# Kernel optimization log

Hardware: AMD Instinct MI355X
Metric: run time of the kernel (lower is better)

Reference implementation:

```python
import jax, jax.numpy as jnp
import numpy as np

B, S, EMB, H = 4, 1024, 1024, 16
HD = EMB // H          # head_dim = 64
MAXP = 512             # RelativePositionalEncoder default max_position


def setup_inputs() -> dict:
    key = jax.random.key(0)
    ks = jax.random.split(key, 13)
    s = 1.0 / np.sqrt(EMB)  # xavier-ish scale keeps softmax logits sane
    return {
        "query": jax.random.normal(ks[0], (B, S, EMB), jnp.float32),
        "key": jax.random.normal(ks[1], (B, S, EMB), jnp.float32),
        "value": jax.random.normal(ks[2], (B, S, EMB), jnp.float32),
        "Wq": jax.random.normal(ks[3], (EMB, EMB), jnp.float32) * s,
        "bq": jnp.zeros((EMB,), jnp.float32),
        "Wk": jax.random.normal(ks[4], (EMB, EMB), jnp.float32) * s,
        "bk": jnp.zeros((EMB,), jnp.float32),
        "Wv": jax.random.normal(ks[5], (EMB, EMB), jnp.float32) * s,
        "bv": jnp.zeros((EMB,), jnp.float32),
        "Wo": jax.random.normal(ks[6], (EMB, EMB), jnp.float32) * s,
        "bo": jnp.zeros((EMB,), jnp.float32),
        "rel_k": jax.random.normal(ks[7], (2 * MAXP + 1, HD), jnp.float32) * 0.05,
        "rel_v": jax.random.normal(ks[8], (2 * MAXP + 1, HD), jnp.float32) * 0.05,
    }


def _split_heads(x):
    # [B,S,E] -> [B,S,H,HD] -> [B,H,S,HD] -> [B*H,S,HD]
    return x.reshape(B, S, H, HD).transpose(0, 2, 1, 3).reshape(B * H, S, HD)


def reference(query, key, value, Wq, bq, Wk, bk, Wv, bv, Wo, bo, rel_k, rel_v):
    scale = jnp.sqrt(jnp.asarray(HD, query.dtype))
    q = _split_heads(query @ Wq + bq)
    k = _split_heads(key @ Wk + bk)
    v = _split_heads(value @ Wv + bv)
    # relative position lookup tables: [Sq, Sk, HD]
    rp = jnp.clip(jnp.arange(S)[None, :] - jnp.arange(S)[:, None], -MAXP, MAXP) + MAXP
    a_key = rel_k[rp]
    a_value = rel_v[rp]
    qk = jnp.einsum('bqd,bkd->bqk', q, k)              # [B*H,S,S]
    rel_qk = jnp.einsum('bqd,qkd->bqk', q, a_key)      # relative score term
    attn = jax.nn.softmax((qk + rel_qk) / scale, axis=-1)
    out = jnp.einsum('bqk,bkd->bqd', attn, v) + jnp.einsum('bqk,qkd->bqd', attn, a_value)
    # faithful to original's view(num_heads, batch, -1, head_dim) then concat reshape
    out = out.reshape(H, B, S, HD).transpose(0, 2, 1, 3).reshape(B, S, H * HD)
    out = out @ Wo + bo
    return (out, attn)
```

## Files before the change

kernel.cpp:

```cpp
#include <hip/hip_runtime.h>


using s16x8 = __attribute__((ext_vector_type(8))) short;
using f32x4 = __attribute__((ext_vector_type(4))) float;

#define MFMA16 __builtin_amdgcn_mfma_f32_16x16x32_bf16

__device__ __forceinline__ float bf2f(unsigned short u) {
  union { unsigned int u; float f; } v; v.u = ((unsigned int)u) << 16; return v.f;
}
__device__ __forceinline__ unsigned short f2bf(float f) {
  union { float f; unsigned int u; } v; v.f = f;
  unsigned int r = (v.u + 0x7FFFu + ((v.u >> 16) & 1u)) >> 16;
  return (unsigned short)r;
}

__global__ __launch_bounds__(256)
void k_prep(const float* __restrict__ Wq, const float* __restrict__ Wk,
            const float* __restrict__ Wv, const float* __restrict__ Wo,
            unsigned short* __restrict__ wqt, unsigned short* __restrict__ wkt,
            unsigned short* __restrict__ wvt, unsigned short* __restrict__ wot,
            const float* __restrict__ rk, const float* __restrict__ rv,
            unsigned short* __restrict__ relkb, unsigned short* __restrict__ rvTb) {
  const int b = blockIdx.x;
  const int tid = threadIdx.x;
  if (b < 4096) {
    __shared__ float t[32][33];
    const int sel = b >> 10, idx = b & 1023;
    const float* W = sel == 0 ? Wq : (sel == 1 ? Wk : (sel == 2 ? Wv : Wo));
    unsigned short* Wt = sel == 0 ? wqt : (sel == 1 ? wkt : (sel == 2 ? wvt : wot));
    const int n0 = (idx & 31) * 32, k0 = (idx >> 5) * 32;
    const int tx = tid & 31, ty = tid >> 5;
#pragma unroll
    for (int r = 0; r < 4; ++r)
      t[ty * 4 + r][tx] = W[(size_t)(k0 + ty * 4 + r) * 1024 + n0 + tx];
    __syncthreads();
#pragma unroll
    for (int r = 0; r < 4; ++r)
      Wt[(size_t)(n0 + ty * 4 + r) * 1024 + k0 + tx] = f2bf(t[tx][ty * 4 + r]);
  } else {
    const int b2 = b - 4096;
    if (b2 < 33) {
      int i = (b2 * 256 + tid) * 8;
      if (i < 65600) {
        float4 a = *(const float4*)(rk + i);
        float4 c = *(const float4*)(rk + i + 4);
        s16x8 o;
        o[0] = (short)f2bf(a.x); o[1] = (short)f2bf(a.y); o[2] = (short)f2bf(a.z); o[3] = (short)f2bf(a.w);
        o[4] = (short)f2bf(c.x); o[5] = (short)f2bf(c.y); o[6] = (short)f2bf(c.z); o[7] = (short)f2bf(c.w);
        *(s16x8*)(relkb + i) = o;
      }
    } else {
      int i = (b2 - 33) * 256 + tid;
      if (i < 65600) {
        int p = i >> 6, d = i & 63;
        rvTb[d * 1040 + p] = f2bf(rv[i]);
      }
    }
  }
}

__global__ __launch_bounds__(256)
void k_trV(const unsigned short* __restrict__ v, unsigned short* __restrict__ vt) {
  __shared__ unsigned short T[64][72];
  const int tid = threadIdx.x;
  const int bh = blockIdx.x >> 4;
  const int s0 = (blockIdx.x & 15) << 6;
  const int r = tid >> 2, cb = (tid & 3) << 4;
  const unsigned short* src = v + ((size_t)bh << 16) + (size_t)(s0 + r) * 64 + cb;
  *(s16x8*)&T[r][cb] = *(const s16x8*)src;
  *(s16x8*)&T[r][cb + 8] = *(const s16x8*)(src + 8);
  __syncthreads();
  unsigned short* dst = vt + ((size_t)bh << 16) + (size_t)r * 1024 + s0 + cb;
  s16x8 o0, o1;
#pragma unroll
  for (int e = 0; e < 8; ++e) o0[e] = T[cb + e][r];
#pragma unroll
  for (int e = 0; e < 8; ++e) o1[e] = T[cb + 8 + e][r];
  *(s16x8*)dst = o0;
  *(s16x8*)(dst + 8) = o1;
}

__global__ __launch_bounds__(256, 2)
void k_gemm_qkv(const float* __restrict__ Aq, const float* __restrict__ Ak, const float* __restrict__ Av,
                const unsigned short* __restrict__ Wq_, const unsigned short* __restrict__ Wk_,
                const unsigned short* __restrict__ Wv_,
                const float* __restrict__ bq_, const float* __restrict__ bk_, const float* __restrict__ bv_,
                unsigned short* __restrict__ Oq, unsigned short* __restrict__ Ok,
                unsigned short* __restrict__ Ov) {
  const int z = blockIdx.z;
  const float* A = z == 0 ? Aq : (z == 1 ? Ak : Av);
  const unsigned short* BT = z == 0 ? Wq_ : (z == 1 ? Wk_ : Wv_);
  const float* bias = z == 0 ? bq_ : (z == 1 ? bk_ : bv_);
  unsigned short* Cout = z == 0 ? Oq : (z == 1 ? Ok : Ov);

  __shared__ alignas(16) unsigned short aT[2][4096];
  __shared__ alignas(16) unsigned short bT[2][2048];
  const int tid = threadIdx.x;
  const int lane = tid & 63;
  const int l15 = lane & 15, lhi = lane >> 4;
  const int w = tid >> 6;
  const int wr = w * 32;
  const int brow = blockIdx.y * 128, bcol = blockIdx.x * 64;
  f32x4 acc[2][4] = {};

  const int c1 = tid, c2 = tid + 256;
  const int r1 = c1 >> 2, kA1 = (c1 & 3) * 8;
  const int r2 = c2 >> 2, kA2 = (c2 & 3) * 8;
  float4 a0, a1, a2, a3;
  s16x8 w1v, w2v;

#define LOADA(kt) do {                                                     \
    const float* p1 = A + (size_t)(brow + r1) * 1024 + (kt) * 32 + kA1;    \
    a0 = *(const float4*)p1; a1 = *(const float4*)(p1 + 4);                \
    const float* p2 = A + (size_t)(brow + r2) * 1024 + (kt) * 32 + kA2;    \
    a2 = *(const float4*)p2; a3 = *(const float4*)(p2 + 4);                \
  } while (0)
#define CVTA() do {                                                        \
    w1v[0] = (short)f2bf(a0.x); w1v[1] = (short)f2bf(a0.y);                \
    w1v[2] = (short)f2bf(a0.z); w1v[3] = (short)f2bf(a0.w);                \
    w1v[4] = (short)f2bf(a1.x); w1v[5] = (short)f2bf(a1.y);                \
    w1v[6] = (short)f2bf(a1.z); w1v[7] = (short)f2bf(a1.w);                \
    w2v[0] = (short)f2bf(a2.x); w2v[1] = (short)f2bf(a2.y);                \
    w2v[2] = (short)f2bf(a2.z); w2v[3] = (short)f2bf(a2.w);                \
    w2v[4] = (short)f2bf(a3.x); w2v[5] = (short)f2bf(a3.y);                \
    w2v[6] = (short)f2bf(a3.z); w2v[7] = (short)f2bf(a3.w);                \
  } while (0)
#define WRA(buf) do {                                                      \
    *(s16x8*)&aT[buf][c1 * 8] = w1v;                                       \
    *(s16x8*)&aT[buf][c2 * 8] = w2v;                                       \
  } while (0)
#define GLB(buf, kt) do {                                                  \
    int row = c1 >> 2, k8 = (c1 & 3) * 8;                                  \
    __builtin_amdgcn_global_load_lds(                                      \
      (const __attribute__((address_space(1))) void*)(BT + (size_t)(bcol + row) * 1024 + (kt) * 32 + k8), \
      (__attribute__((address_space(3))) void*)(&bT[buf][c1 * 8]), 16, 0, 0); \
  } while (0)

  LOADA(0); GLB(0, 0); CVTA(); WRA(0);
  int cur = 0;
  for (int kt = 0; kt < 32; ++kt) {
    __syncthreads();
    if (kt + 1 < 32) { LOADA(kt + 1); GLB(cur ^ 1, kt + 1); }
    s16x8 af[2], bfv[4];
#pragma unroll
    for (int m = 0; m < 2; ++m)
      af[m] = *(const s16x8*)&aT[cur][(wr + m * 16 + l15) * 32 + lhi * 8];
#pragma unroll
    for (int n = 0; n < 4; ++n)
      bfv[n] = *(const s16x8*)&bT[cur][(n * 16 + l15) * 32 + lhi * 8];
#pragma unroll
    for (int m = 0; m < 2; ++m)
#pragma unroll
      for (int n = 0; n < 4; ++n)
        acc[m][n] = MFMA16(af[m], bfv[n], acc[m][n], 0, 0, 0);
    if (kt + 1 < 32) { CVTA(); WRA(cur ^ 1); }
    __syncthreads();
    cur ^= 1;
  }
#undef LOADA
#undef CVTA
#undef WRA
#undef GLB

#pragma unroll
  for (int m = 0; m < 2; ++m) {
#pragma unroll
    for (int n = 0; n < 4; ++n) {
      int col = bcol + n * 16 + l15;
      float bs = bias[col];
#pragma unroll
      for (int j = 0; j < 4; ++j) {
        int r = brow + wr + m * 16 + lhi * 4 + j;
        float v = acc[m][n][j] + bs;
        int bb = r >> 10, s = r & 1023, h = col >> 6, d = col & 63;
        Cout[(((size_t)((bb << 4) + h) * 1024 + s) << 6) + d] = f2bf(v);
      }
    }
  }
}

__global__ __launch_bounds__(256, 2)
void k_gemm_o(const unsigned short* __restrict__ A, const unsigned short* __restrict__ BT,
              const float* __restrict__ bias, float* __restrict__ Cout) {
  __shared__ alignas(16) unsigned short aT[2][4096];
  __shared__ alignas(16) unsigned short bT[2][2048];
  const int tid = threadIdx.x;
  const int lane = tid & 63;
  const int l15 = lane & 15, lhi = lane >> 4;
  const int w = tid >> 6;
  const int wr = w * 32;
  const int brow = blockIdx.y * 128, bcol = blockIdx.x * 64;
  f32x4 acc[2][4] = {};

#define STAGE(buf, kt) do {                                                              \
    int k0s = (kt) * 32;                                                                 \
    {                                                                                    \
      int c = tid;                                                                       \
      int row = c >> 2, k8 = (c & 3) * 8;                                                \
      __builtin_amdgcn_global_load_lds(                                                  \
        (const __attribute__((address_space(1))) void*)(A + (size_t)(brow + row) * 1024 + k0s + k8), \
        (__attribute__((address_space(3))) void*)(&aT[buf][c * 8]), 16, 0, 0);           \
      __builtin_amdgcn_global_load_lds(                                                  \
        (const __attribute__((address_space(1))) void*)(BT + (size_t)(bcol + row) * 1024 + k0s + k8),\
        (__attribute__((address_space(3))) void*)(&bT[buf][c * 8]), 16, 0, 0);           \
    }                                                                                    \
    {                                                                                    \
      int c = tid + 256;                                                                 \
      int row = c >> 2, k8 = (c & 3) * 8;                                                \
      __builtin_amdgcn_global_load_lds(                                                  \
        (const __attribute__((address_space(1))) void*)(A + (size_t)(brow + row) * 1024 + k0s + k8), \
        (__attribute__((address_space(3))) void*)(&aT[buf][c * 8]), 16, 0, 0);           \
    }                                                                                    \
  } while (0)

  int cur = 0;
  STAGE(0, 0);
  for (int kt = 0; kt < 32; ++kt) {
    __syncthreads();
    if (kt + 1 < 32) STAGE(cur ^ 1, kt + 1);
    s16x8 af[2], bfv[4];
#pragma unroll
    for (int m = 0; m < 2; ++m)
      af[m] = *(const s16x8*)&aT[cur][(wr + m * 16 + l15) * 32 + lhi * 8];
#pragma unroll
    for (int n = 0; n < 4; ++n)
      bfv[n] = *(const s16x8*)&bT[cur][(n * 16 + l15) * 32 + lhi * 8];
#pragma unroll
    for (int m = 0; m < 2; ++m)
#pragma unroll
      for (int n = 0; n < 4; ++n)
        acc[m][n] = MFMA16(af[m], bfv[n], acc[m][n], 0, 0, 0);
    __syncthreads();
    cur ^= 1;
  }
#undef STAGE

#pragma unroll
  for (int m = 0; m < 2; ++m) {
#pragma unroll
    for (int n = 0; n < 4; ++n) {
      int col = bcol + n * 16 + l15;
      float bs = bias[col];
#pragma unroll
      for (int j = 0; j < 4; ++j) {
        int r = brow + wr + m * 16 + lhi * 4 + j;
        Cout[(size_t)r * 1024 + col] = acc[m][n][j] + bs;
      }
    }
  }
}

#define RPW 1032
#define PWP 520

__global__ __launch_bounds__(512, 5)
void k_attn(const unsigned short* __restrict__ qb, const unsigned short* __restrict__ kbm,
            const unsigned short* __restrict__ vT, const unsigned short* __restrict__ relk,
            const unsigned short* __restrict__ rvT, float* __restrict__ attn_out,
            unsigned short* __restrict__ xscr) {
  __shared__ alignas(16) unsigned short pbuf[16 * RPW];
  __shared__ alignas(16) unsigned short TbPw[16 * PWP];
  __shared__ float red[8][16];
  __shared__ float izS[16], plS[16], phS[16];

  const int tid = threadIdx.x;
  const int lane = tid & 63;
  const int w = tid >> 6;
  const int l15 = lane & 15, lhi = lane >> 4;
  const int orig = ((blockIdx.x & 7) << 9) | (blockIdx.x >> 3);
  const int bh = orig >> 6;
  const int q0 = (orig & 63) << 4;

  const unsigned short* Qh = qb + ((size_t)bh << 16);
  const unsigned short* Kh = kbm + ((size_t)bh << 16);
  const unsigned short* Vth = vT + ((size_t)bh << 16);

  const unsigned short* qp = Qh + (size_t)(q0 + l15) * 64 + lhi * 8;
  s16x8 qa0 = *(const s16x8*)qp;
  s16x8 qa1 = *(const s16x8*)(qp + 32);

  float zp = 0.f;
  for (int half = 0; half < 2; ++half) {
    const int khalf = half << 9;
    __syncthreads();

    {
      const int PT0 = ((khalf - q0 + 497) >> 4) << 4;
      const int PT1 = khalf - q0 + 1023;
      for (int pt = PT0 + w * 16; pt <= PT1; pt += 128) {
        int pr = pt + l15; pr = pr < 0 ? 0 : (pr > 1024 ? 1024 : pr);
        const unsigned short* rp = relk + (size_t)pr * 64 + lhi * 8;
        s16x8 rf0 = *(const s16x8*)rp;
        s16x8 rf1 = *(const s16x8*)(rp + 32);
        f32x4 d = {0.f, 0.f, 0.f, 0.f};
        d = MFMA16(qa0, rf0, d, 0, 0, 0);
        d = MFMA16(qa1, rf1, d, 0, 0, 0);
#pragma unroll
        for (int j = 0; j < 4; ++j) {
          int qi = lhi * 4 + j;
          int u = pt + l15 - khalf + q0 + qi - 512;
          if (u >= 0 && u < 512) TbPw[qi * PWP + u] = f2bf(d[j]);
        }
      }
    }
    __syncthreads();

    const unsigned short* kbp = Kh + (size_t)(khalf + w * 16 + l15) * 64 + lhi * 8;
    s16x8 ka0 = *(const s16x8*)kbp;
    s16x8 ka1 = *(const s16x8*)(kbp + 32);
    s16x8 kb0 = *(const s16x8*)(kbp + 128 * 64);
    s16x8 kb1 = *(const s16x8*)(kbp + 128 * 64 + 32);
#pragma unroll
    for (int n = 0; n < 4; ++n) {
      const int ktile = khalf + w * 16 + n * 128;
      s16x8 kf0 = (n & 1) ? kb0 : ka0;
      s16x8 kf1 = (n & 1) ? kb1 : ka1;
      f32x4 c = {0.f, 0.f, 0.f, 0.f};
      __builtin_amdgcn_s_setprio(1);
      c = MFMA16(kf0, qa0, c, 0, 0, 0);
      c = MFMA16(kf1, qa1, c, 0, 0, 0);
      __builtin_amdgcn_s_setprio(0);
      if (n < 2) {
        const unsigned short* np = kbp + (n + 2) * 128 * 64;
        if (n & 1) { kb0 = *(const s16x8*)np; kb1 = *(const s16x8*)(np + 32); }
        else       { ka0 = *(const s16x8*)np; ka1 = *(const s16x8*)(np + 32); }
      }
      uint2 tv = *(const uint2*)&TbPw[l15 * PWP + (ktile - khalf) + lhi * 4];
      float t0 = bf2f((unsigned short)(tv.x & 0xFFFF));
      float t1 = bf2f((unsigned short)(tv.x >> 16));
      float t2 = bf2f((unsigned short)(tv.y & 0xFFFF));
      float t3 = bf2f((unsigned short)(tv.y >> 16));
      float e0 = __expf((c[0] + t0) * 0.125f);
      float e1 = __expf((c[1] + t1) * 0.125f);
      float e2 = __expf((c[2] + t2) * 0.125f);
      float e3 = __expf((c[3] + t3) * 0.125f);
      zp += (e0 + e1) + (e2 + e3);
      uint2 pk;
      pk.x = (unsigned int)f2bf(e0) | ((unsigned int)f2bf(e1) << 16);
      pk.y = (unsigned int)f2bf(e2) | ((unsigned int)f2bf(e3) << 16);
      *(uint2*)&pbuf[l15 * RPW + ktile + lhi * 4] = pk;
    }
  }

  zp += __shfl_xor(zp, 16, 64);
  zp += __shfl_xor(zp, 32, 64);
  if (lane < 16) red[w][lane] = zp;
  __syncthreads();
  if (tid < 16) {
    float s = 0.f;
#pragma unroll
    for (int ww = 0; ww < 8; ++ww) s += red[ww][tid];
    izS[tid] = 1.0f / s;
  }

  {
    const int qi = tid >> 5, tq = tid & 31;
    const int qa = q0 + qi;
    int lo, hi;
    const bool isPh = (qa < 512);
    if (isPh) { lo = qa + 512; hi = 1024; }
    else      { lo = 0;        hi = qa - 511; }
    float s = 0.f;
    const unsigned short* srow = pbuf + qi * RPW;
    const int kb0i = lo & ~7;
    for (int k8 = kb0i + tq * 8; k8 < hi; k8 += 256) {
      s16x8 v8 = *(const s16x8*)&srow[k8];
#pragma unroll
      for (int e = 0; e < 8; ++e) {
        int k = k8 + e;
        s += (k >= lo && k < hi) ? bf2f((unsigned short)v8[e]) : 0.f;
      }
    }
#pragma unroll
    for (int off = 1; off < 32; off <<= 1) s += __shfl_xor(s, off, 64);
    if (tq == 0) { plS[qi] = isPh ? 0.f : s; phS[qi] = isPh ? s : 0.f; }
  }
  __syncthreads();

  {
    float* ao = attn_out + ((size_t)bh << 20) + ((size_t)q0 << 10);
#pragma unroll
    for (int n = 0; n < 4; ++n) {
      int idx = n * 512 + tid;
      int row = idx >> 7, c8 = (idx & 127) << 3;
      float iz = izS[row];
      s16x8 p8 = *(const s16x8*)&pbuf[row * RPW + c8];
      f32x4 o0, o1;
      o0[0] = bf2f((unsigned short)p8[0]) * iz; o0[1] = bf2f((unsigned short)p8[1]) * iz;
      o0[2] = bf2f((unsigned short)p8[2]) * iz; o0[3] = bf2f((unsigned short)p8[3]) * iz;
      o1[0] = bf2f((unsigned short)p8[4]) * iz; o1[1] = bf2f((unsigned short)p8[5]) * iz;
      o1[2] = bf2f((unsigned short)p8[6]) * iz; o1[3] = bf2f((unsigned short)p8[7]) * iz;
      __builtin_nontemporal_store(o0, (f32x4*)(ao + (row << 10) + c8));
      __builtin_nontemporal_store(o1, (f32x4*)(ao + (row << 10) + c8 + 4));
    }
  }

  f32x4 acc = {0.f, 0.f, 0.f, 0.f};
  const int d0 = (w >> 1) << 4;
  const int kbase = (w & 1) << 9;
  const unsigned short* vrow = Vth + (size_t)(d0 + l15) * 1024 + lhi * 8;
#pragma unroll 8
  for (int kc = kbase; kc < kbase + 512; kc += 32) {
    s16x8 pa = *(const s16x8*)&pbuf[l15 * RPW + kc + lhi * 8];
    s16x8 vf = *(const s16x8*)(vrow + kc);
    acc = MFMA16(pa, vf, acc, 0, 0, 0);
  }

  const unsigned short* rrow = rvT + (size_t)(d0 + l15) * 1040 + lhi * 8;
  {
    const int sqi = tid >> 5, stq = tid & 31;
    const int ssh = sqi & 7, shs = ssh >> 1;
    const bool sodd = (ssh & 1) != 0;
    unsigned short* drow = TbPw + sqi * PWP;
    const unsigned short* srow = pbuf + sqi * RPW;
    const int kq = (w & 1) << 8;
    for (int ph = 0; ph < 2; ++ph) {
      __syncthreads();
      const int base = q0 + sqi + (ph ? 0 : -512);
      for (int t = stq; t < 64; t += 32) {
        const int kw0 = base + t * 8;
        s16x8 o;
        if (kw0 >= 0 && kw0 + 8 <= 1024) {
          const int A = kw0 - ssh;
          union { s16x8 v; unsigned int u[4]; } a0u, a1u, ov;
          a0u.v = *(const s16x8*)&srow[A];
          a1u.v = *(const s16x8*)&srow[A + 8];
          unsigned int wd[8];
#pragma unroll
          for (int j2 = 0; j2 < 4; ++j2) { wd[j2] = a0u.u[j2]; wd[4 + j2] = a1u.u[j2]; }
          unsigned int v7[7];
#pragma unroll
          for (int j2 = 0; j2 < 7; ++j2) {
            unsigned int sf = (wd[j2] >> 16) | (wd[j2 + 1] << 16);
            v7[j2] = sodd ? sf : wd[j2];
          }
#pragma unroll
          for (int j2 = 0; j2 < 4; ++j2) {
            unsigned int t0 = (shs & 1) ? v7[j2 + 1] : v7[j2];
            unsigned int t1 = (shs & 1) ? v7[j2 + 3] : v7[j2 + 2];
            ov.u[j2] = (shs & 2) ? t1 : t0;
          }
          o = ov.v;
        } else if (kw0 + 8 <= 0 || kw0 >= 1024) {
          o = (s16x8){0, 0, 0, 0, 0, 0, 0, 0};
        } else {
#pragma unroll
          for (int e = 0; e < 8; ++e) {
            int k = kw0 + e;
            int kc2 = k < 0 ? 0 : (k > 1023 ? 1023 : k);
            unsigned short vv = srow[kc2];
            o[e] = (k >= 0 && k < 1024) ? (short)vv : (short)0;
          }
        }
        *(s16x8*)&drow[t * 8] = o;
        if (ph == 0 && t == 0) drow[0] = f2bf(plS[sqi]);
      }
      __syncthreads();
#pragma unroll 8
      for (int kc = kq; kc < kq + 256; kc += 32) {
        s16x8 pa = *(const s16x8*)&TbPw[l15 * PWP + kc + lhi * 8];
        s16x8 rb = *(const s16x8*)(rrow + (ph << 9) + kc);
        acc = MFMA16(pa, rb, acc, 0, 0, 0);
      }
    }
  }

  __syncthreads();
  float* fscr = (float*)TbPw;
  if (w & 1) {
    f32x4* dst = (f32x4*)&fscr[(((w >> 1) << 6) | lane) << 2];
    *dst = acc;
  }
  __syncthreads();
  if (!(w & 1)) {
    f32x4 other = *(const f32x4*)&fscr[(((w >> 1) << 6) | lane) << 2];
    float rv1024 = bf2f(rvT[(size_t)(d0 + l15) * 1040 + 1024]);
    const size_t fb = ((size_t)(bh >> 2) << 18) + ((size_t)(bh & 3) << 6);
#pragma unroll
    for (int j = 0; j < 4; ++j) {
      int qi = lhi * 4 + j;
      float v = (acc[j] + other[j] + phS[qi] * rv1024) * izS[qi];
      xscr[fb + ((size_t)(q0 + qi) << 8) + d0 + l15] = f2bf(v);
    }
  }
}

extern "C" void kernel_launch(void* const* d_in, const int* in_sizes, int n_in,
                              void* d_out, int out_size, void* d_ws, size_t ws_size,
                              hipStream_t stream) {
  (void)in_sizes; (void)n_in; (void)out_size; (void)ws_size;
  const float* query = (const float*)d_in[0];
  const float* key   = (const float*)d_in[1];
  const float* value = (const float*)d_in[2];
  const float* Wq = (const float*)d_in[3];
  const float* bq = (const float*)d_in[4];
  const float* Wk = (const float*)d_in[5];
  const float* bk = (const float*)d_in[6];
  const float* Wv = (const float*)d_in[7];
  const float* bv = (const float*)d_in[8];
  const float* Wo = (const float*)d_in[9];
  const float* bo = (const float*)d_in[10];
  const float* rel_k = (const float*)d_in[11];
  const float* rel_v = (const float*)d_in[12];

  char* ws = (char*)d_ws;
  const size_t MB = 1024 * 1024;
  unsigned short* qb    = (unsigned short*)(ws);
  unsigned short* kbuf  = (unsigned short*)(ws + 8 * MB);
  unsigned short* vbuf  = (unsigned short*)(ws + 16 * MB);
  unsigned short* vTb   = (unsigned short*)(ws + 24 * MB);
  unsigned short* wqt   = (unsigned short*)(ws + 32 * MB);
  unsigned short* wkt   = (unsigned short*)(ws + 34 * MB);
  unsigned short* wvt   = (unsigned short*)(ws + 36 * MB);
  unsigned short* wot   = (unsigned short*)(ws + 38 * MB);
  unsigned short* relkb = (unsigned short*)(ws + 40 * MB);
  unsigned short* rvTb  = (unsigned short*)(ws + 40 * MB + 256 * 1024);
  unsigned short* xscr  = vbuf;

  float* out0 = (float*)d_out;
  float* attn_out = out0 + 4194304;

  k_prep<<<4386, 256, 0, stream>>>(Wq, Wk, Wv, Wo, wqt, wkt, wvt, wot,
                                   rel_k, rel_v, relkb, rvTb);

  k_gemm_qkv<<<dim3(16, 32, 3), 256, 0, stream>>>(query, key, value,
                                                  wqt, wkt, wvt,
                                                  bq, bk, bv,
                                                  qb, kbuf, vbuf);

  k_trV<<<1024, 256, 0, stream>>>(vbuf, vTb);

  k_attn<<<4096, 512, 0, stream>>>(qb, kbuf, vTb, relkb, rvTb, attn_out, xscr);

  k_gemm_o<<<dim3(16, 32), 256, 0, stream>>>(xscr, wot, bo, out0);
}
```

Before: 365.4 us.

## Split fused attention kernel into score/softmax and PV kernels via global attn

```diff
diff --git a/kernel.cpp b/kernel.cpp
--- a/kernel.cpp
+++ b/kernel.cpp
@@ -254,14 +254,13 @@
 #define RPW 1032
 #define PWP 520
 
-__global__ __launch_bounds__(512, 5)
-void k_attn(const unsigned short* __restrict__ qb, const unsigned short* __restrict__ kbm,
-            const unsigned short* __restrict__ vT, const unsigned short* __restrict__ relk,
-            const unsigned short* __restrict__ rvT, float* __restrict__ attn_out,
-            unsigned short* __restrict__ xscr) {
+__global__ __launch_bounds__(256, 2)
+void k_score(const unsigned short* __restrict__ qb, const unsigned short* __restrict__ kbm,
+             const unsigned short* __restrict__ relk, float* __restrict__ attn_out,
+             float* __restrict__ plN, float* __restrict__ phN) {
   __shared__ alignas(16) unsigned short pbuf[16 * RPW];
   __shared__ alignas(16) unsigned short TbPw[16 * PWP];
-  __shared__ float red[8][16];
+  __shared__ float red[4][16];
   __shared__ float izS[16], plS[16], phS[16];
 
   const int tid = threadIdx.x;
@@ -274,7 +273,6 @@
 
   const unsigned short* Qh = qb + ((size_t)bh << 16);
   const unsigned short* Kh = kbm + ((size_t)bh << 16);
-  const unsigned short* Vth = vT + ((size_t)bh << 16);
 
   const unsigned short* qp = Qh + (size_t)(q0 + l15) * 64 + lhi * 8;
   s16x8 qa0 = *(const s16x8*)qp;
@@ -288,7 +286,7 @@
     {
       const int PT0 = ((khalf - q0 + 497) >> 4) << 4;
       const int PT1 = khalf - q0 + 1023;
-      for (int pt = PT0 + w * 16; pt <= PT1; pt += 128) {
+      for (int pt = PT0 + w * 16; pt <= PT1; pt += 64) {
         int pr = pt + l15; pr = pr < 0 ? 0 : (pr > 1024 ? 1024 : pr);
         const unsigned short* rp = relk + (size_t)pr * 64 + lhi * 8;
         s16x8 rf0 = *(const s16x8*)rp;
@@ -307,39 +305,38 @@
     __syncthreads();
 
     const unsigned short* kbp = Kh + (size_t)(khalf + w * 16 + l15) * 64 + lhi * 8;
-    s16x8 ka0 = *(const s16x8*)kbp;
-    s16x8 ka1 = *(const s16x8*)(kbp + 32);
-    s16x8 kb0 = *(const s16x8*)(kbp + 128 * 64);
-    s16x8 kb1 = *(const s16x8*)(kbp + 128 * 64 + 32);
-#pragma unroll
-    for (int n = 0; n < 4; ++n) {
-      const int ktile = khalf + w * 16 + n * 128;
-      s16x8 kf0 = (n & 1) ? kb0 : ka0;
-      s16x8 kf1 = (n & 1) ? kb1 : ka1;
-      f32x4 c = {0.f, 0.f, 0.f, 0.f};
-      __builtin_amdgcn_s_setprio(1);
-      c = MFMA16(kf0, qa0, c, 0, 0, 0);
-      c = MFMA16(kf1, qa1, c, 0, 0, 0);
-      __builtin_amdgcn_s_setprio(0);
-      if (n < 2) {
-        const unsigned short* np = kbp + (n + 2) * 128 * 64;
-        if (n & 1) { kb0 = *(const s16x8*)np; kb1 = *(const s16x8*)(np + 32); }
-        else       { ka0 = *(const s16x8*)np; ka1 = *(const s16x8*)(np + 32); }
-      }
-      uint2 tv = *(const uint2*)&TbPw[l15 * PWP + (ktile - khalf) + lhi * 4];
-      float t0 = bf2f((unsigned short)(tv.x & 0xFFFF));
-      float t1 = bf2f((unsigned short)(tv.x >> 16));
-      float t2 = bf2f((unsigned short)(tv.y & 0xFFFF));
-      float t3 = bf2f((unsigned short)(tv.y >> 16));
-      float e0 = __expf((c[0] + t0) * 0.125f);
-      float e1 = __expf((c[1] + t1) * 0.125f);
-      float e2 = __expf((c[2] + t2) * 0.125f);
-      float e3 = __expf((c[3] + t3) * 0.125f);
-      zp += (e0 + e1) + (e2 + e3);
-      uint2 pk;
-      pk.x = (unsigned int)f2bf(e0) | ((unsigned int)f2bf(e1) << 16);
-      pk.y = (unsigned int)f2bf(e2) | ((unsigned int)f2bf(e3) << 16);
-      *(uint2*)&pbuf[l15 * RPW + ktile + lhi * 4] = pk;
+#pragma unroll
+    for (int g = 0; g < 2; ++g) {
+      s16x8 kf0[4], kf1[4];
+#pragma unroll
+      for (int n = 0; n < 4; ++n) {
+        const unsigned short* p = kbp + (size_t)(g * 4 + n) * 4096;
+        kf0[n] = *(const s16x8*)p;
+        kf1[n] = *(const s16x8*)(p + 32);
+      }
+#pragma unroll
+      for (int n = 0; n < 4; ++n) {
+        const int ktile = khalf + w * 16 + (g * 4 + n) * 64;
+        f32x4 c = {0.f, 0.f, 0.f, 0.f};
+        __builtin_amdgcn_s_setprio(1);
+        c = MFMA16(kf0[n], qa0, c, 0, 0, 0);
+        c = MFMA16(kf1[n], qa1, c, 0, 0, 0);
+        __builtin_amdgcn_s_setprio(0);
+        uint2 tv = *(const uint2*)&TbPw[l15 * PWP + (ktile - khalf) + lhi * 4];
+        float t0 = bf2f((unsigned short)(tv.x & 0xFFFF));
+        float t1 = bf2f((unsigned short)(tv.x >> 16));
+        float t2 = bf2f((unsigned short)(tv.y & 0xFFFF));
+        float t3 = bf2f((unsigned short)(tv.y >> 16));
+        float e0 = __expf((c[0] + t0) * 0.125f);
+        float e1 = __expf((c[1] + t1) * 0.125f);
+        float e2 = __expf((c[2] + t2) * 0.125f);
+        float e3 = __expf((c[3] + t3) * 0.125f);
+        zp += (e0 + e1) + (e2 + e3);
+        uint2 pk;
+        pk.x = (unsigned int)f2bf(e0) | ((unsigned int)f2bf(e1) << 16);
+        pk.y = (unsigned int)f2bf(e2) | ((unsigned int)f2bf(e3) << 16);
+        *(uint2*)&pbuf[l15 * RPW + ktile + lhi * 4] = pk;
+      }
     }
   }
 
@@ -347,15 +344,11 @@
   zp += __shfl_xor(zp, 32, 64);
   if (lane < 16) red[w][lane] = zp;
   __syncthreads();
-  if (tid < 16) {
-    float s = 0.f;
-#pragma unroll
-    for (int ww = 0; ww < 8; ++ww) s += red[ww][tid];
-    izS[tid] = 1.0f / s;
-  }
+  if (tid < 16)
+    izS[tid] = 1.0f / (red[0][tid] + red[1][tid] + red[2][tid] + red[3][tid]);
 
   {
-    const int qi = tid >> 5, tq = tid & 31;
+    const int qi = tid >> 4, tq = tid & 15;
     const int qa = q0 + qi;
     int lo, hi;
     const bool isPh = (qa < 512);
@@ -363,8 +356,8 @@
     else      { lo = 0;        hi = qa - 511; }
     float s = 0.f;
     const unsigned short* srow = pbuf + qi * RPW;
-    const int kb0i = lo & ~7;
-    for (int k8 = kb0i + tq * 8; k8 < hi; k8 += 256) {
+    const int kb0 = lo & ~7;
+    for (int k8 = kb0 + tq * 8; k8 < hi; k8 += 128) {
       s16x8 v8 = *(const s16x8*)&srow[k8];
 #pragma unroll
       for (int e = 0; e < 8; ++e) {
@@ -373,17 +366,22 @@
       }
     }
 #pragma unroll
-    for (int off = 1; off < 32; off <<= 1) s += __shfl_xor(s, off, 64);
+    for (int off = 1; off < 16; off <<= 1) s += __shfl_xor(s, off, 64);
     if (tq == 0) { plS[qi] = isPh ? 0.f : s; phS[qi] = isPh ? s : 0.f; }
   }
   __syncthreads();
+
+  if (tid < 16) {
+    plN[(bh << 10) + q0 + tid] = plS[tid] * izS[tid];
+    phN[(bh << 10) + q0 + tid] = phS[tid] * izS[tid];
+  }
 
   {
     float* ao = attn_out + ((size_t)bh << 20) + ((size_t)q0 << 10);
 #pragma unroll
-    for (int n = 0; n < 4; ++n) {
-      int idx = n * 512 + tid;
-      int row = idx >> 7, c8 = (idx & 127) << 3;
+    for (int n = 0; n < 8; ++n) {
+      int row = (tid >> 7) + n * 2;
+      int c8 = (tid & 127) << 3;
       float iz = izS[row];
       s16x8 p8 = *(const s16x8*)&pbuf[row * RPW + c8];
       f32x4 o0, o1;
@@ -395,94 +393,75 @@
       __builtin_nontemporal_store(o1, (f32x4*)(ao + (row << 10) + c8 + 4));
     }
   }
+}
+
+__global__ __launch_bounds__(256)
+void k_pv(const float* __restrict__ attn, const unsigned short* __restrict__ vT,
+          const unsigned short* __restrict__ rvT, const float* __restrict__ plN,
+          const float* __restrict__ phN, unsigned short* __restrict__ xscr) {
+  const int tid = threadIdx.x;
+  const int lane = tid & 63;
+  const int w = tid >> 6;
+  const int l15 = lane & 15, lhi = lane >> 4;
+  const int orig = ((blockIdx.x & 7) << 9) | (blockIdx.x >> 3);
+  const int bh = orig >> 6;
+  const int q0 = (orig & 63) << 4;
+  const int d0 = w << 4;
+
+  const float* arow = attn + ((size_t)bh << 20) + ((size_t)(q0 + l15) << 10);
+  const unsigned short* vrow = vT + ((size_t)bh << 16) + (size_t)(d0 + l15) * 1024 + lhi * 8;
+  const unsigned short* rrow = rvT + (size_t)(d0 + l15) * 1040 + lhi * 8;
 
   f32x4 acc = {0.f, 0.f, 0.f, 0.f};
-  const int d0 = (w >> 1) << 4;
-  const int kbase = (w & 1) << 9;
-  const unsigned short* vrow = Vth + (size_t)(d0 + l15) * 1024 + lhi * 8;
-#pragma unroll 8
-  for (int kc = kbase; kc < kbase + 512; kc += 32) {
-    s16x8 pa = *(const s16x8*)&pbuf[l15 * RPW + kc + lhi * 8];
+
+#pragma unroll 4
+  for (int kc = 0; kc < 1024; kc += 32) {
+    float4 a = *(const float4*)(arow + kc + lhi * 8);
+    float4 b = *(const float4*)(arow + kc + lhi * 8 + 4);
+    union { s16x8 v; unsigned int u[4]; } pa;
+    asm("v_cvt_pk_bf16_f32 %0, %1, %2" : "=v"(pa.u[0]) : "v"(a.x), "v"(a.y));
+    asm("v_cvt_pk_bf16_f32 %0, %1, %2" : "=v"(pa.u[1]) : "v"(a.z), "v"(a.w));
+    asm("v_cvt_pk_bf16_f32 %0, %1, %2" : "=v"(pa.u[2]) : "v"(b.x), "v"(b.y));
+    asm("v_cvt_pk_bf16_f32 %0, %1, %2" : "=v"(pa.u[3]) : "v"(b.z), "v"(b.w));
     s16x8 vf = *(const s16x8*)(vrow + kc);
-    acc = MFMA16(pa, vf, acc, 0, 0, 0);
-  }
-
-  const unsigned short* rrow = rvT + (size_t)(d0 + l15) * 1040 + lhi * 8;
-  {
-    const int sqi = tid >> 5, stq = tid & 31;
-    const int ssh = sqi & 7, shs = ssh >> 1;
-    const bool sodd = (ssh & 1) != 0;
-    unsigned short* drow = TbPw + sqi * PWP;
-    const unsigned short* srow = pbuf + sqi * RPW;
-    const int kq = (w & 1) << 8;
-    for (int ph = 0; ph < 2; ++ph) {
-      __syncthreads();
-      const int base = q0 + sqi + (ph ? 0 : -512);
-      for (int t = stq; t < 64; t += 32) {
-        const int kw0 = base + t * 8;
-        s16x8 o;
-        if (kw0 >= 0 && kw0 + 8 <= 1024) {
-          const int A = kw0 - ssh;
-          union { s16x8 v; unsigned int u[4]; } a0u, a1u, ov;
-          a0u.v = *(const s16x8*)&srow[A];
-          a1u.v = *(const s16x8*)&srow[A + 8];
-          unsigned int wd[8];
-#pragma unroll
-          for (int j2 = 0; j2 < 4; ++j2) { wd[j2] = a0u.u[j2]; wd[4 + j2] = a1u.u[j2]; }
-          unsigned int v7[7];
-#pragma unroll
-          for (int j2 = 0; j2 < 7; ++j2) {
-            unsigned int sf = (wd[j2] >> 16) | (wd[j2 + 1] << 16);
-            v7[j2] = sodd ? sf : wd[j2];
-          }
-#pragma unroll
-          for (int j2 = 0; j2 < 4; ++j2) {
-            unsigned int t0 = (shs & 1) ? v7[j2 + 1] : v7[j2];
-            unsigned int t1 = (shs & 1) ? v7[j2 + 3] : v7[j2 + 2];
-            ov.u[j2] = (shs & 2) ? t1 : t0;
-          }
-          o = ov.v;
-        } else if (kw0 + 8 <= 0 || kw0 >= 1024) {
-          o = (s16x8){0, 0, 0, 0, 0, 0, 0, 0};
-        } else {
-#pragma unroll
-          for (int e = 0; e < 8; ++e) {
-            int k = kw0 + e;
-            int kc2 = k < 0 ? 0 : (k > 1023 ? 1023 : k);
-            unsigned short vv = srow[kc2];
-            o[e] = (k >= 0 && k < 1024) ? (short)vv : (short)0;
-          }
-        }
-        *(s16x8*)&drow[t * 8] = o;
-        if (ph == 0 && t == 0) drow[0] = f2bf(plS[sqi]);
-      }
-      __syncthreads();
-#pragma unroll 8
-      for (int kc = kq; kc < kq + 256; kc += 32) {
-        s16x8 pa = *(const s16x8*)&TbPw[l15 * PWP + kc + lhi * 8];
-        s16x8 rb = *(const s16x8*)(rrow + (ph << 9) + kc);
-        acc = MFMA16(pa, rb, acc, 0, 0, 0);
-      }
-    }
-  }
-
-  __syncthreads();
-  float* fscr = (float*)TbPw;
-  if (w & 1) {
-    f32x4* dst = (f32x4*)&fscr[(((w >> 1) << 6) | lane) << 2];
-    *dst = acc;
-  }
-  __syncthreads();
-  if (!(w & 1)) {
-    f32x4 other = *(const f32x4*)&fscr[(((w >> 1) << 6) | lane) << 2];
-    float rv1024 = bf2f(rvT[(size_t)(d0 + l15) * 1040 + 1024]);
-    const size_t fb = ((size_t)(bh >> 2) << 18) + ((size_t)(bh & 3) << 6);
-#pragma unroll
-    for (int j = 0; j < 4; ++j) {
-      int qi = lhi * 4 + j;
-      float v = (acc[j] + other[j] + phS[qi] * rv1024) * izS[qi];
-      xscr[fb + ((size_t)(q0 + qi) << 8) + d0 + l15] = f2bf(v);
-    }
+    acc = MFMA16(pa.v, vf, acc, 0, 0, 0);
+  }
+
+  const float pl = plN[(bh << 10) + q0 + l15];
+#pragma unroll 4
+  for (int uc = 0; uc < 1024; uc += 32) {
+    const int k0 = q0 + l15 + uc + lhi * 8 - 512;
+    union { s16x8 v; unsigned int u[4]; } wa;
+    if (k0 >= 0 && k0 + 8 <= 1024) {
+      float4 a = *(const float4*)(arow + k0);
+      float4 b = *(const float4*)(arow + k0 + 4);
+      asm("v_cvt_pk_bf16_f32 %0, %1, %2" : "=v"(wa.u[0]) : "v"(a.x), "v"(a.y));
+      asm("v_cvt_pk_bf16_f32 %0, %1, %2" : "=v"(wa.u[1]) : "v"(a.z), "v"(a.w));
+      asm("v_cvt_pk_bf16_f32 %0, %1, %2" : "=v"(wa.u[2]) : "v"(b.x), "v"(b.y));
+      asm("v_cvt_pk_bf16_f32 %0, %1, %2" : "=v"(wa.u[3]) : "v"(b.z), "v"(b.w));
+    } else if (k0 + 8 <= 0 || k0 >= 1024) {
+      wa.v = (s16x8){0, 0, 0, 0, 0, 0, 0, 0};
+    } else {
+#pragma unroll
+      for (int e = 0; e < 8; ++e) {
+        int k = k0 + e;
+        int kc2 = k < 0 ? 0 : (k > 1023 ? 1023 : k);
+        float pv = arow[kc2];
+        wa.v[e] = (k >= 0 && k < 1024) ? (short)f2bf(pv) : (short)0;
+      }
+    }
+    if (uc == 0 && lhi == 0) wa.v[0] = (short)f2bf(pl);
+    s16x8 rb = *(const s16x8*)(rrow + uc);
+    acc = MFMA16(wa.v, rb, acc, 0, 0, 0);
+  }
+
+  const float rv1024 = bf2f(rvT[(size_t)(d0 + l15) * 1040 + 1024]);
+  const size_t fb = ((size_t)(bh >> 2) << 18) + ((size_t)(bh & 3) << 6);
+#pragma unroll
+  for (int j = 0; j < 4; ++j) {
+    int qi = lhi * 4 + j;
+    float v = acc[j] + phN[(bh << 10) + q0 + qi] * rv1024;
+    xscr[fb + ((size_t)(q0 + qi) << 8) + d0 + l15] = f2bf(v);
   }
 }
 
@@ -516,6 +495,8 @@
   unsigned short* wot   = (unsigned short*)(ws + 38 * MB);
   unsigned short* relkb = (unsigned short*)(ws + 40 * MB);
   unsigned short* rvTb  = (unsigned short*)(ws + 40 * MB + 256 * 1024);
+  float* plN            = (float*)(ws + 40 * MB + 512 * 1024);
+  float* phN            = (float*)(ws + 40 * MB + 768 * 1024);
   unsigned short* xscr  = vbuf;
 
   float* out0 = (float*)d_out;
@@ -531,7 +512,9 @@
 
   k_trV<<<1024, 256, 0, stream>>>(vbuf, vTb);
 
-  k_attn<<<4096, 512, 0, stream>>>(qb, kbuf, vTb, relkb, rvTb, attn_out, xscr);
+  k_score<<<4096, 256, 0, stream>>>(qb, kbuf, relkb, attn_out, plN, phN);
+
+  k_pv<<<4096, 256, 0, stream>>>(attn_out, vTb, rvTb, plN, phN, xscr);
 
   k_gemm_o<<<dim3(16, 32), 256, 0, stream>>>(xscr, wot, bo, out0);
 }
```

After: 556.5 us. 52.3% more time.

## Halve attention block to four waves, each covering full key range

Applied to the files above, without the earlier changes.

```diff
diff --git a/kernel.cpp b/kernel.cpp
--- a/kernel.cpp
+++ b/kernel.cpp
@@ -254,14 +254,14 @@
 #define RPW 1032
 #define PWP 520
 
-__global__ __launch_bounds__(512, 5)
+__global__ __launch_bounds__(256, 3)
 void k_attn(const unsigned short* __restrict__ qb, const unsigned short* __restrict__ kbm,
             const unsigned short* __restrict__ vT, const unsigned short* __restrict__ relk,
             const unsigned short* __restrict__ rvT, float* __restrict__ attn_out,
             unsigned short* __restrict__ xscr) {
   __shared__ alignas(16) unsigned short pbuf[16 * RPW];
   __shared__ alignas(16) unsigned short TbPw[16 * PWP];
-  __shared__ float red[8][16];
+  __shared__ float red[4][16];
   __shared__ float izS[16], plS[16], phS[16];
 
   const int tid = threadIdx.x;
@@ -288,7 +288,7 @@
     {
       const int PT0 = ((khalf - q0 + 497) >> 4) << 4;
       const int PT1 = khalf - q0 + 1023;
-      for (int pt = PT0 + w * 16; pt <= PT1; pt += 128) {
+      for (int pt = PT0 + w * 16; pt <= PT1; pt += 64) {
         int pr = pt + l15; pr = pr < 0 ? 0 : (pr > 1024 ? 1024 : pr);
         const unsigned short* rp = relk + (size_t)pr * 64 + lhi * 8;
         s16x8 rf0 = *(const s16x8*)rp;
@@ -307,39 +307,38 @@
     __syncthreads();
 
     const unsigned short* kbp = Kh + (size_t)(khalf + w * 16 + l15) * 64 + lhi * 8;
-    s16x8 ka0 = *(const s16x8*)kbp;
-    s16x8 ka1 = *(const s16x8*)(kbp + 32);
-    s16x8 kb0 = *(const s16x8*)(kbp + 128 * 64);
-    s16x8 kb1 = *(const s16x8*)(kbp + 128 * 64 + 32);
-#pragma unroll
-    for (int n = 0; n < 4; ++n) {
-      const int ktile = khalf + w * 16 + n * 128;
-      s16x8 kf0 = (n & 1) ? kb0 : ka0;
-      s16x8 kf1 = (n & 1) ? kb1 : ka1;
-      f32x4 c = {0.f, 0.f, 0.f, 0.f};
-      __builtin_amdgcn_s_setprio(1);
-      c = MFMA16(kf0, qa0, c, 0, 0, 0);
-      c = MFMA16(kf1, qa1, c, 0, 0, 0);
-      __builtin_amdgcn_s_setprio(0);
-      if (n < 2) {
-        const unsigned short* np = kbp + (n + 2) * 128 * 64;
-        if (n & 1) { kb0 = *(const s16x8*)np; kb1 = *(const s16x8*)(np + 32); }
-        else       { ka0 = *(const s16x8*)np; ka1 = *(const s16x8*)(np + 32); }
-      }
-      uint2 tv = *(const uint2*)&TbPw[l15 * PWP + (ktile - khalf) + lhi * 4];
-      float t0 = bf2f((unsigned short)(tv.x & 0xFFFF));
-      float t1 = bf2f((unsigned short)(tv.x >> 16));
-      float t2 = bf2f((unsigned short)(tv.y & 0xFFFF));
-      float t3 = bf2f((unsigned short)(tv.y >> 16));
-      float e0 = __expf((c[0] + t0) * 0.125f);
-      float e1 = __expf((c[1] + t1) * 0.125f);
-      float e2 = __expf((c[2] + t2) * 0.125f);
-      float e3 = __expf((c[3] + t3) * 0.125f);
-      zp += (e0 + e1) + (e2 + e3);
-      uint2 pk;
-      pk.x = (unsigned int)f2bf(e0) | ((unsigned int)f2bf(e1) << 16);
-      pk.y = (unsigned int)f2bf(e2) | ((unsigned int)f2bf(e3) << 16);
-      *(uint2*)&pbuf[l15 * RPW + ktile + lhi * 4] = pk;
+#pragma unroll
+    for (int g = 0; g < 2; ++g) {
+      s16x8 kf0[4], kf1[4];
+#pragma unroll
+      for (int n = 0; n < 4; ++n) {
+        const unsigned short* p = kbp + (size_t)(g * 4 + n) * 4096;
+        kf0[n] = *(const s16x8*)p;
+        kf1[n] = *(const s16x8*)(p + 32);
+      }
+#pragma unroll
+      for (int n = 0; n < 4; ++n) {
+        const int ktile = khalf + w * 16 + (g * 4 + n) * 64;
+        f32x4 c = {0.f, 0.f, 0.f, 0.f};
+        __builtin_amdgcn_s_setprio(1);
+        c = MFMA16(kf0[n], qa0, c, 0, 0, 0);
+        c = MFMA16(kf1[n], qa1, c, 0, 0, 0);
+        __builtin_amdgcn_s_setprio(0);
+        uint2 tv = *(const uint2*)&TbPw[l15 * PWP + (ktile - khalf) + lhi * 4];
+        float t0 = bf2f((unsigned short)(tv.x & 0xFFFF));
+        float t1 = bf2f((unsigned short)(tv.x >> 16));
+        float t2 = bf2f((unsigned short)(tv.y & 0xFFFF));
+        float t3 = bf2f((unsigned short)(tv.y >> 16));
+        float e0 = __expf((c[0] + t0) * 0.125f);
+        float e1 = __expf((c[1] + t1) * 0.125f);
+        float e2 = __expf((c[2] + t2) * 0.125f);
+        float e3 = __expf((c[3] + t3) * 0.125f);
+        zp += (e0 + e1) + (e2 + e3);
+        uint2 pk;
+        pk.x = (unsigned int)f2bf(e0) | ((unsigned int)f2bf(e1) << 16);
+        pk.y = (unsigned int)f2bf(e2) | ((unsigned int)f2bf(e3) << 16);
+        *(uint2*)&pbuf[l15 * RPW + ktile + lhi * 4] = pk;
+      }
     }
   }
 
@@ -347,15 +346,11 @@
   zp += __shfl_xor(zp, 32, 64);
   if (lane < 16) red[w][lane] = zp;
   __syncthreads();
-  if (tid < 16) {
-    float s = 0.f;
-#pragma unroll
-    for (int ww = 0; ww < 8; ++ww) s += red[ww][tid];
-    izS[tid] = 1.0f / s;
-  }
+  if (tid < 16)
+    izS[tid] = 1.0f / (red[0][tid] + red[1][tid] + red[2][tid] + red[3][tid]);
 
   {
-    const int qi = tid >> 5, tq = tid & 31;
+    const int qi = tid >> 4, tq = tid & 15;
     const int qa = q0 + qi;
     int lo, hi;
     const bool isPh = (qa < 512);
@@ -363,8 +358,8 @@
     else      { lo = 0;        hi = qa - 511; }
     float s = 0.f;
     const unsigned short* srow = pbuf + qi * RPW;
-    const int kb0i = lo & ~7;
-    for (int k8 = kb0i + tq * 8; k8 < hi; k8 += 256) {
+    const int kb0 = lo & ~7;
+    for (int k8 = kb0 + tq * 8; k8 < hi; k8 += 128) {
       s16x8 v8 = *(const s16x8*)&srow[k8];
 #pragma unroll
       for (int e = 0; e < 8; ++e) {
@@ -373,7 +368,7 @@
       }
     }
 #pragma unroll
-    for (int off = 1; off < 32; off <<= 1) s += __shfl_xor(s, off, 64);
+    for (int off = 1; off < 16; off <<= 1) s += __shfl_xor(s, off, 64);
     if (tq == 0) { plS[qi] = isPh ? 0.f : s; phS[qi] = isPh ? s : 0.f; }
   }
   __syncthreads();
@@ -381,9 +376,9 @@
   {
     float* ao = attn_out + ((size_t)bh << 20) + ((size_t)q0 << 10);
 #pragma unroll
-    for (int n = 0; n < 4; ++n) {
-      int idx = n * 512 + tid;
-      int row = idx >> 7, c8 = (idx & 127) << 3;
+    for (int n = 0; n < 8; ++n) {
+      int row = (tid >> 7) + n * 2;
+      int c8 = (tid & 127) << 3;
       float iz = izS[row];
       s16x8 p8 = *(const s16x8*)&pbuf[row * RPW + c8];
       f32x4 o0, o1;
@@ -397,28 +392,26 @@
   }
 
   f32x4 acc = {0.f, 0.f, 0.f, 0.f};
-  const int d0 = (w >> 1) << 4;
-  const int kbase = (w & 1) << 9;
-  const unsigned short* vrow = Vth + (size_t)(d0 + l15) * 1024 + lhi * 8;
+  const int d0w = w << 4;
+  const unsigned short* vrow = Vth + (size_t)(d0w + l15) * 1024 + lhi * 8;
 #pragma unroll 8
-  for (int kc = kbase; kc < kbase + 512; kc += 32) {
+  for (int kc = 0; kc < 1024; kc += 32) {
     s16x8 pa = *(const s16x8*)&pbuf[l15 * RPW + kc + lhi * 8];
     s16x8 vf = *(const s16x8*)(vrow + kc);
     acc = MFMA16(pa, vf, acc, 0, 0, 0);
   }
 
-  const unsigned short* rrow = rvT + (size_t)(d0 + l15) * 1040 + lhi * 8;
+  const unsigned short* rrow = rvT + (size_t)(d0w + l15) * 1040 + lhi * 8;
   {
-    const int sqi = tid >> 5, stq = tid & 31;
+    const int sqi = tid >> 4, stq = tid & 15;
     const int ssh = sqi & 7, shs = ssh >> 1;
     const bool sodd = (ssh & 1) != 0;
     unsigned short* drow = TbPw + sqi * PWP;
     const unsigned short* srow = pbuf + sqi * RPW;
-    const int kq = (w & 1) << 8;
     for (int ph = 0; ph < 2; ++ph) {
       __syncthreads();
       const int base = q0 + sqi + (ph ? 0 : -512);
-      for (int t = stq; t < 64; t += 32) {
+      for (int t = stq; t < 64; t += 16) {
         const int kw0 = base + t * 8;
         s16x8 o;
         if (kw0 >= 0 && kw0 + 8 <= 1024) {
@@ -458,7 +451,7 @@
       }
       __syncthreads();
 #pragma unroll 8
-      for (int kc = kq; kc < kq + 256; kc += 32) {
+      for (int kc = 0; kc < 512; kc += 32) {
         s16x8 pa = *(const s16x8*)&TbPw[l15 * PWP + kc + lhi * 8];
         s16x8 rb = *(const s16x8*)(rrow + (ph << 9) + kc);
         acc = MFMA16(pa, rb, acc, 0, 0, 0);
@@ -466,23 +459,13 @@
     }
   }
 
-  __syncthreads();
-  float* fscr = (float*)TbPw;
-  if (w & 1) {
-    f32x4* dst = (f32x4*)&fscr[(((w >> 1) << 6) | lane) << 2];
-    *dst = acc;
-  }
-  __syncthreads();
-  if (!(w & 1)) {
-    f32x4 other = *(const f32x4*)&fscr[(((w >> 1) << 6) | lane) << 2];
-    float rv1024 = bf2f(rvT[(size_t)(d0 + l15) * 1040 + 1024]);
-    const size_t fb = ((size_t)(bh >> 2) << 18) + ((size_t)(bh & 3) << 6);
-#pragma unroll
-    for (int j = 0; j < 4; ++j) {
-      int qi = lhi * 4 + j;
-      float v = (acc[j] + other[j] + phS[qi] * rv1024) * izS[qi];
-      xscr[fb + ((size_t)(q0 + qi) << 8) + d0 + l15] = f2bf(v);
-    }
+  float rv1024 = bf2f(rvT[(size_t)(d0w + l15) * 1040 + 1024]);
+  const size_t fb = ((size_t)(bh >> 2) << 18) + ((size_t)(bh & 3) << 6);
+#pragma unroll
+  for (int j = 0; j < 4; ++j) {
+    int qi = lhi * 4 + j;
+    float v = (acc[j] + phS[qi] * rv1024) * izS[qi];
+    xscr[fb + ((size_t)(q0 + qi) << 8) + d0w + l15] = f2bf(v);
   }
 }
 
@@ -531,7 +514,7 @@
 
   k_trV<<<1024, 256, 0, stream>>>(vbuf, vTb);
 
-  k_attn<<<4096, 512, 0, stream>>>(qb, kbuf, vTb, relkb, rvTb, attn_out, xscr);
+  k_attn<<<4096, 256, 0, stream>>>(qb, kbuf, vTb, relkb, rvTb, attn_out, xscr);
 
   k_gemm_o<<<dim3(16, 32), 256, 0, stream>>>(xscr, wot, bo, out0);
 }
```

Result: faster. 338.8 us (-7.3%).
